# Performance work log

Hardware: AMD Instinct MI355X
Metric: run time of the kernel (lower is better)

## Reference

```python
import jax, jax.numpy as jnp
import numpy as np

NEG_INF = -1e9
B, Q, M, D, H = 8, 512, 512, 1024, 16
S = D // H  # size per head


def rel_shift(x):
    # x: [B, H, Q, R] -> TransformerXL relative shift
    b, h, q, r = x.shape
    x = jnp.pad(x, ((0, 0), (0, 0), (0, 0), (1, 0)))
    x = x.reshape(b, h, r + 1, q)[:, :, 1:, :]
    return x.reshape(b, h, q, r)


def setup_inputs() -> dict:
    key = jax.random.key(0)
    ks = jax.random.split(key, 10)
    query_seqs = jax.random.normal(ks[0], (B, Q, D), jnp.float32)
    memory_seqs = jax.random.normal(ks[1], (B, M, D), jnp.float32)
    positional_encoding = jax.random.normal(ks[2], (Q + M, D), jnp.float32)
    # causal mask over concatenated [memory | query]: query token i may attend
    # to all memory tokens and query tokens <= i. 1 = masked.
    q_idx = jnp.arange(Q)[:, None]
    r_idx = jnp.arange(Q + M)[None, :]
    token_mask = (r_idx > q_idx + M).astype(jnp.float32)[None, None]  # [1,1,Q,Q+M]
    std = 0.02
    Wq = jax.random.normal(ks[3], (D, H, S), jnp.float32) * std
    Wk = jax.random.normal(ks[4], (D, H, S), jnp.float32) * std
    Wv = jax.random.normal(ks[5], (D, H, S), jnp.float32) * std
    Wr = jax.random.normal(ks[6], (D, H, S), jnp.float32) * std
    Wo = jax.random.normal(ks[7], (H, S, D), jnp.float32) * std
    content_bias = jax.random.normal(ks[8], (H, S), jnp.float32) * std
    position_bias = jax.random.normal(ks[9], (H, S), jnp.float32) * std
    return dict(query_seqs=query_seqs, memory_seqs=memory_seqs,
                positional_encoding=positional_encoding, token_mask=token_mask,
                Wq=Wq, Wk=Wk, Wv=Wv, Wr=Wr, Wo=Wo,
                content_bias=content_bias, position_bias=position_bias)


def reference(query_seqs, memory_seqs, positional_encoding, token_mask,
              Wq, Wk, Wv, Wr, Wo, content_bias, position_bias):
    # reference = [memory | query] along time axis
    reference_seqs = jnp.concatenate([memory_seqs, query_seqs], axis=1)  # [B,R,D]
    q = jnp.einsum('bqd,dhs->bqhs', query_seqs, Wq)       # [B,Q,H,S]
    k = jnp.einsum('brd,dhs->brhs', reference_seqs, Wk)   # [B,R,H,S]
    v = jnp.einsum('brd,dhs->brhs', reference_seqs, Wv)   # [B,R,H,S]
    r = jnp.einsum('rd,dhs->rhs', positional_encoding, Wr)  # [R,H,S]

    content = jnp.einsum('bqhs,brhs->bhqr', q + content_bias, k)
    positions = jnp.einsum('bqhs,rhs->bhqr', q + position_bias, r)
    positions = rel_shift(positions)

    logits = (content + positions) / jnp.sqrt(jnp.float32(S))
    logits = logits + token_mask * NEG_INF
    attn = jax.nn.softmax(logits, axis=3)  # dropout disabled (inference)

    out = jnp.einsum('bhqr,brhs->bqhs', attn, v)
    return jnp.einsum('bqhs,hsd->bqd', out, Wo)
```

## Files before the change

kernel.cpp:

```cpp
#include <hip/hip_runtime.h>

typedef _Float16 f16;
typedef _Float16 f16x8 __attribute__((ext_vector_type(8)));
typedef float f32x4 __attribute__((ext_vector_type(4)));

#define MFMA_F16(a, b, c) __builtin_amdgcn_mfma_f32_16x16x32_f16((a), (b), (c), 0, 0, 0)

#define SCL 0.125f

__device__ __forceinline__ void gl_lds16(const void* g, void* l) {
    __builtin_amdgcn_global_load_lds((const __attribute__((address_space(1))) unsigned int*)g,
                                     (__attribute__((address_space(3))) unsigned int*)l, 16, 0, 0);
}

__global__ void prep(const float* __restrict__ q, const float* __restrict__ mem,
                     const float* __restrict__ Wq, const float* __restrict__ Wk,
                     const float* __restrict__ Wv, const float* __restrict__ Wr,
                     const float* __restrict__ Wo,
                     f16* __restrict__ wt, f16* __restrict__ ref16)
{
    __shared__ float t[32][33];
    const int bid = blockIdx.x, tid = threadIdx.x;
    if (bid < 5120) {
        const int wi = bid >> 10, tt = bid & 1023;
        const float* src;
        switch (wi) { case 0: src = Wq; break; case 1: src = Wk; break;
                      case 2: src = Wv; break; case 3: src = Wr; break; default: src = Wo; }
        f16* dst = wt + ((size_t)wi << 20);
        const int x = (tt & 31) * 32, y = (tt >> 5) * 32;
        const int tx = tid & 31, ty = tid >> 5;
#pragma unroll
        for (int k2 = 0; k2 < 4; ++k2)
            t[ty + k2 * 8][tx] = src[(size_t)(y + ty + k2 * 8) * 1024 + x + tx];
        __syncthreads();
#pragma unroll
        for (int k2 = 0; k2 < 4; ++k2)
            dst[(size_t)(x + ty + k2 * 8) * 1024 + y + tx] = (f16)t[tx][ty + k2 * 8];
    } else {
        const int idx = (bid - 5120) * 256 + tid;
        const int half = idx >> 19;
        const int c = idx & 0x7FFFF;
        const int b = c >> 16, i = (c >> 7) & 511, ch = c & 127;
        const float* src = (half == 0 ? q : mem) + (((size_t)(b * 512 + i)) << 10) + ch * 8;
        const int t2 = (half == 0) ? (512 + i) : i;
        f16* dst = ref16 + ((((size_t)b << 10) + t2) << 10) + ch * 8;
        const float4 f0 = reinterpret_cast<const float4*>(src)[0];
        const float4 f1 = reinterpret_cast<const float4*>(src)[1];
        f16x8 v;
        v[0] = (f16)f0.x; v[1] = (f16)f0.y; v[2] = (f16)f0.z; v[3] = (f16)f0.w;
        v[4] = (f16)f1.x; v[5] = (f16)f1.y; v[6] = (f16)f1.z; v[7] = (f16)f1.w;
        *reinterpret_cast<f16x8*>(dst) = v;
    }
}

__global__ __launch_bounds__(256, 4)
void proj_kernel(const f16* __restrict__ ref16, const float* __restrict__ posenc,
                 const f16* __restrict__ wts,
                 f16* __restrict__ qc16, f16* __restrict__ qp16,
                 f16* __restrict__ k16, f16* __restrict__ vT16, f16* __restrict__ r16,
                 const float* __restrict__ cb, const float* __restrict__ pbias)
{
    __shared__ __align__(16) f16 SH[16384];
    f16* At = SH;
    f16* Bt = SH + 8192;

    const int tid = threadIdx.x, lane = tid & 63, w = tid >> 6;
    const int wr = w >> 1, wc = w & 1;

    const int bid = blockIdx.x;
    int mode, local, perx, shf;
    if (bid < 256)       { mode = 0; local = bid;        perx = 4; shf = 2; }
    else if (bid < 768)  { mode = 1; local = bid - 256;  perx = 8; shf = 3; }
    else if (bid < 1280) { mode = 2; local = bid - 768;  perx = 8; shf = 3; }
    else                 { mode = 3; local = bid - 1280; perx = 1; shf = 0; }
    const int xcd = local & 7, m = local >> 3;
    const int rt = xcd * perx + (m & (perx - 1));
    const int ct = m >> shf;
    const int i0 = rt * 128, n0 = ct * 128;
    const f16* BT = wts + ((size_t)mode << 20);

    f32x4 acc[4][4] = {};

    for (int ks = 0; ks < 16; ++ks) {
        const int k0 = ks * 64;
#pragma unroll
        for (int it = 0; it < 4; ++it) {
            const int c = tid + it * 256;
            const int row = c >> 3, ch = c & 7, chs = ch ^ (row & 7);
            const int grow = i0 + row;
            char* lA = reinterpret_cast<char*>(At) + ((c & ~63) << 4);
            char* lB = reinterpret_cast<char*>(Bt) + ((c & ~63) << 4);
            if (mode == 3) {
                const float* sr = posenc + (size_t)grow * 1024 + k0 + ch * 8;
                const float4 f0 = reinterpret_cast<const float4*>(sr)[0];
                const float4 f1 = reinterpret_cast<const float4*>(sr)[1];
                f16x8 av;
                av[0] = (f16)f0.x; av[1] = (f16)f0.y; av[2] = (f16)f0.z; av[3] = (f16)f0.w;
                av[4] = (f16)f1.x; av[5] = (f16)f1.y; av[6] = (f16)f1.z; av[7] = (f16)f1.w;
                *reinterpret_cast<f16x8*>(reinterpret_cast<char*>(At) + row * 128 + (chs << 4)) = av;
            } else {
                const size_t arow = (mode == 0) ? (size_t)((grow >> 9) * 1024 + 512 + (grow & 511))
                                                : (size_t)grow;
                gl_lds16(ref16 + arow * 1024 + k0 + chs * 8, lA);
            }
            gl_lds16(BT + (size_t)(n0 + row) * 1024 + k0 + chs * 8, lB);
        }
        __syncthreads();
#pragma unroll
        for (int kk = 0; kk < 2; ++kk) {
            f16x8 avf[4], bvf[4];
            const int chh = kk * 4 + (lane >> 4);
#pragma unroll
            for (int mi = 0; mi < 4; ++mi) {
                const int row = wr * 64 + mi * 16 + (lane & 15);
                avf[mi] = *reinterpret_cast<const f16x8*>(reinterpret_cast<char*>(At) + row * 128 + ((chh ^ (row & 7)) << 4));
            }
#pragma unroll
            for (int n = 0; n < 4; ++n) {
                const int row = wc * 64 + n * 16 + (lane & 15);
                bvf[n] = *reinterpret_cast<const f16x8*>(reinterpret_cast<char*>(Bt) + row * 128 + ((chh ^ (row & 7)) << 4));
            }
#pragma unroll
            for (int mi = 0; mi < 4; ++mi)
#pragma unroll
                for (int n = 0; n < 4; ++n)
                    acc[mi][n] = MFMA_F16(avf[mi], bvf[n], acc[mi][n]);
        }
        __syncthreads();
    }

    if (mode == 2) {
#pragma unroll
        for (int mi = 0; mi < 4; ++mi)
#pragma unroll
            for (int n = 0; n < 4; ++n)
#pragma unroll
                for (int rg = 0; rg < 4; ++rg) {
                    const int jl = wr * 64 + mi * 16 + (lane >> 4) * 4 + rg;
                    const int cl = wc * 64 + n * 16 + (lane & 15);
                    SH[cl * 128 + jl] = (f16)acc[mi][n][rg];
                }
        __syncthreads();
        const int b = i0 >> 10;
        const int j0l = i0 & 1023;
#pragma unroll
        for (int it = 0; it < 8; ++it) {
            const int c = tid + it * 256;
            const int cl = c >> 4, ch = c & 15;
            const int col = n0 + cl;
            const int h = col >> 6, s = col & 63;
            f16* dst = vT16 + (((size_t)(b * 16 + h) * 64 + s) * 1024 + j0l + ch * 8);
            *reinterpret_cast<f16x8*>(dst) = *reinterpret_cast<const f16x8*>(SH + cl * 128 + ch * 8);
        }
    } else {
#pragma unroll
        for (int mi = 0; mi < 4; ++mi)
#pragma unroll
            for (int n = 0; n < 4; ++n)
#pragma unroll
                for (int rg = 0; rg < 4; ++rg) {
                    const int row = i0 + wr * 64 + mi * 16 + (lane >> 4) * 4 + rg;
                    const int col = n0 + wc * 64 + n * 16 + (lane & 15);
                    const float v = acc[mi][n][rg];
                    if (mode == 0) {
                        const int b = row >> 9, i = row & 511, h = col >> 6, s = col & 63;
                        const size_t idx = (((size_t)(b * 16 + h) * 512) + i) * 64 + s;
                        qc16[idx] = (f16)((v + cb[col]) * SCL);
                        qp16[idx] = (f16)((v + pbias[col]) * SCL);
                    } else if (mode == 1) {
                        const int b = row >> 10, j = row & 1023, h = col >> 6, s = col & 63;
                        k16[(((size_t)(b * 16 + h) * 1024) + j) * 64 + s] = (f16)v;
                    } else {
                        const int h = col >> 6, s = col & 63;
                        r16[((size_t)h * 1024 + row) * 64 + s] = (f16)v;
                    }
                }
    }
}

__global__ __launch_bounds__(256, 4)
void oproj_kernel(const f16* __restrict__ ao16, const f16* __restrict__ WoT, float* __restrict__ out)
{
    __shared__ __align__(16) f16 SH[16384];
    f16* At = SH;
    f16* Bt = SH + 8192;
    const int tid = threadIdx.x, lane = tid & 63, w = tid >> 6;
    const int wr = w >> 1, wc = w & 1;
    const int xcd = blockIdx.x & 7, m = blockIdx.x >> 3;
    const int rt = xcd * 4 + (m & 3), ct = m >> 2;
    const int i0 = rt * 128, n0 = ct * 128;

    f32x4 acc[4][4] = {};
    for (int ks = 0; ks < 16; ++ks) {
        const int k0 = ks * 64;
#pragma unroll
        for (int it = 0; it < 4; ++it) {
            const int c = tid + it * 256;
            const int row = c >> 3, ch = c & 7, chs = ch ^ (row & 7);
            char* lA = reinterpret_cast<char*>(At) + ((c & ~63) << 4);
            char* lB = reinterpret_cast<char*>(Bt) + ((c & ~63) << 4);
            gl_lds16(ao16 + (size_t)(i0 + row) * 1024 + k0 + chs * 8, lA);
            gl_lds16(WoT + (size_t)(n0 + row) * 1024 + k0 + chs * 8, lB);
        }
        __syncthreads();
#pragma unroll
        for (int kk = 0; kk < 2; ++kk) {
            f16x8 avf[4], bvf[4];
            const int chh = kk * 4 + (lane >> 4);
#pragma unroll
            for (int mi = 0; mi < 4; ++mi) {
                const int row = wr * 64 + mi * 16 + (lane & 15);
                avf[mi] = *reinterpret_cast<const f16x8*>(reinterpret_cast<char*>(At) + row * 128 + ((chh ^ (row & 7)) << 4));
            }
#pragma unroll
            for (int n = 0; n < 4; ++n) {
                const int row = wc * 64 + n * 16 + (lane & 15);
                bvf[n] = *reinterpret_cast<const f16x8*>(reinterpret_cast<char*>(Bt) + row * 128 + ((chh ^ (row & 7)) << 4));
            }
#pragma unroll
            for (int mi = 0; mi < 4; ++mi)
#pragma unroll
                for (int n = 0; n < 4; ++n)
                    acc[mi][n] = MFMA_F16(avf[mi], bvf[n], acc[mi][n]);
        }
        __syncthreads();
    }
#pragma unroll
    for (int mi = 0; mi < 4; ++mi)
#pragma unroll
        for (int n = 0; n < 4; ++n)
#pragma unroll
            for (int rg = 0; rg < 4; ++rg) {
                const int row = i0 + wr * 64 + mi * 16 + (lane >> 4) * 4 + rg;
                const int col = n0 + wc * 64 + n * 16 + (lane & 15);
                out[(size_t)row * 1024 + col] = acc[mi][n][rg];
            }
}

__global__ __launch_bounds__(512, 4)
void attn_kernel(const f16* __restrict__ qc16, const f16* __restrict__ qp16,
                 const f16* __restrict__ k16, const f16* __restrict__ vT16,
                 const f16* __restrict__ r16, f16* __restrict__ attnout)
{
    __shared__ __align__(16) f16 KT[4096], VT[4096], RT[4096];
    __shared__ __align__(16) f16 PR[128 * 68];
    __shared__ __align__(16) f16 PB[8 * 2 * 16 * 68];

    const int tid = threadIdx.x, lane = tid & 63, w = tid >> 6;
    const int n = blockIdx.x;
    const int xcd = n & 7, m = n >> 3;
    const int h = xcd + 8 * (m >> 5);
    const int b = (m >> 2) & 7;
    const int iB = m & 3;
    const int i0 = iB * 128;
    const int bh = b * 16 + h;

    const f16* kbase = k16 + (size_t)bh * 1024 * 64;
    const f16* vbase = vT16 + (size_t)bh * 64 * 1024;
    const f16* rbase = r16 + (size_t)h * 1024 * 64;

    f16x8 qcf[2], qpf[2];
    {
        const size_t qoff = ((size_t)bh * 512 + i0 + w * 16 + (lane & 15)) * 64;
#pragma unroll
        for (int kk = 0; kk < 2; ++kk) {
            const int ch = (kk * 4 + (lane >> 4)) * 8;
            qcf[kk] = *reinterpret_cast<const f16x8*>(qc16 + qoff + ch);
            qpf[kk] = *reinterpret_cast<const f16x8*>(qp16 + qoff + ch);
        }
    }

    auto stage64 = [&](f16* dst, const f16* src, int rowstride) {
        const int row = tid >> 3, ch = tid & 7, chs = ch ^ (row & 7);
        gl_lds16(src + (size_t)row * rowstride + chs * 8,
                 reinterpret_cast<char*>(dst) + ((tid & ~63) << 4));
    };

    auto compute_pblock = [&](int bt) {
        const int slot = bt & 1;
        f32x4 pc[4] = {};
#pragma unroll
        for (int kk = 0; kk < 2; ++kk) {
            const int chh = kk * 4 + (lane >> 4);
#pragma unroll
            for (int tf = 0; tf < 4; ++tf) {
                const int brow = tf * 16 + (lane & 15);
                const f16x8 rv = *reinterpret_cast<const f16x8*>(reinterpret_cast<char*>(RT) + brow * 128 + ((chh ^ (brow & 7)) << 4));
                pc[tf] = MFMA_F16(qpf[kk], rv, pc[tf]);
            }
        }
        f16* pbw = PB + (size_t)((w * 2 + slot) * 16) * 68;
#pragma unroll
        for (int tf = 0; tf < 4; ++tf)
#pragma unroll
            for (int rg = 0; rg < 4; ++rg) {
                const int r = (lane >> 4) * 4 + rg;
                pbw[r * 68 + tf * 16 + (lane & 15)] = (f16)pc[tf][rg];
            }
    };

    {
        const int bt0 = 6 - 2 * iB;
        stage64(RT, rbase + (size_t)(bt0 * 64) * 64, 64);
        __syncthreads();
        compute_pblock(bt0);
        __syncthreads();
        stage64(RT, rbase + (size_t)((bt0 + 1) * 64) * 64, 64);
        __syncthreads();
        compute_pblock(bt0 + 1);
    }

    float mrun[4] = {-1e30f, -1e30f, -1e30f, -1e30f};
    float lrun[4] = {0.f, 0.f, 0.f, 0.f};
    f32x4 o[4] = {};

    const int njt = 2 * iB + 10;
    for (int jt = 0; jt < njt; ++jt) {
        const int j0 = jt * 64;
        const int bt = jt - 2 * iB + 8;
        __syncthreads();
        stage64(KT, kbase + (size_t)j0 * 64, 64);
        stage64(VT, vbase + j0, 1024);
        if (bt <= 15) stage64(RT, rbase + (size_t)(bt * 64) * 64, 64);
        __syncthreads();

        if (w < 4 && bt <= 15) compute_pblock(bt);

        f32x4 cfr[4] = {};
        __builtin_amdgcn_s_setprio(1);
#pragma unroll
        for (int kk = 0; kk < 2; ++kk) {
            const int chh = kk * 4 + (lane >> 4);
#pragma unroll
            for (int jf = 0; jf < 4; ++jf) {
                const int brow = jf * 16 + (lane & 15);
                const f16x8 kv = *reinterpret_cast<const f16x8*>(reinterpret_cast<char*>(KT) + brow * 128 + ((chh ^ (brow & 7)) << 4));
                cfr[jf] = MFMA_F16(qcf[kk], kv, cfr[jf]);
            }
        }
        __builtin_amdgcn_s_setprio(0);

        const int tb = j0 + 511 - i0 - w * 16;
        float lg[4][4];
#pragma unroll
        for (int jf = 0; jf < 4; ++jf)
#pragma unroll
            for (int rg = 0; rg < 4; ++rg) {
                const int il = (lane >> 4) * 4 + rg;
                const int t = tb + jf * 16 + (lane & 15) - il;
                const float pv = (float)PB[(size_t)((w * 2 + ((t >> 6) & 1)) * 16 + il) * 68 + (t & 63)];
                lg[jf][rg] = (t <= 1023) ? (cfr[jf][rg] + pv) : -1e30f;
            }

        float mx[4];
#pragma unroll
        for (int rg = 0; rg < 4; ++rg) {
            float v = fmaxf(fmaxf(lg[0][rg], lg[1][rg]), fmaxf(lg[2][rg], lg[3][rg]));
#pragma unroll
            for (int d = 1; d < 16; d <<= 1) v = fmaxf(v, __shfl_xor(v, d));
            mx[rg] = v;
        }
        const float need = fmaxf(fmaxf(mx[0] - mrun[0], mx[1] - mrun[1]),
                                 fmaxf(mx[2] - mrun[2], mx[3] - mrun[3]));
        if (__all(need <= 8.0f)) {
#pragma unroll
            for (int rg = 0; rg < 4; ++rg) {
                float rs = 0.f;
                const int il = w * 16 + (lane >> 4) * 4 + rg;
#pragma unroll
                for (int jf = 0; jf < 4; ++jf) {
                    const float p = __expf(lg[jf][rg] - mrun[rg]);
                    rs += p;
                    PR[il * 68 + jf * 16 + (lane & 15)] = (f16)p;
                }
#pragma unroll
                for (int d = 1; d < 16; d <<= 1) rs += __shfl_xor(rs, d);
                lrun[rg] += rs;
            }
        } else {
#pragma unroll
            for (int rg = 0; rg < 4; ++rg) {
                const float mnew = fmaxf(mrun[rg], mx[rg]);
                const float al = __expf(mrun[rg] - mnew);
                mrun[rg] = mnew;
                float rs = 0.f;
                const int il = w * 16 + (lane >> 4) * 4 + rg;
#pragma unroll
                for (int jf = 0; jf < 4; ++jf) {
                    const float p = __expf(lg[jf][rg] - mnew);
                    rs += p;
                    PR[il * 68 + jf * 16 + (lane & 15)] = (f16)p;
                }
#pragma unroll
                for (int d = 1; d < 16; d <<= 1) rs += __shfl_xor(rs, d);
                lrun[rg] = lrun[rg] * al + rs;
#pragma unroll
                for (int sf = 0; sf < 4; ++sf) o[sf][rg] *= al;
            }
        }

        __builtin_amdgcn_s_setprio(1);
#pragma unroll
        for (int kk = 0; kk < 2; ++kk) {
            const int chh = kk * 4 + (lane >> 4);
            const int arow = w * 16 + (lane & 15);
            const f16x8 ap = *reinterpret_cast<const f16x8*>(reinterpret_cast<char*>(PR) + arow * 136 + chh * 16);
#pragma unroll
            for (int sf = 0; sf < 4; ++sf) {
                const int brow = sf * 16 + (lane & 15);
                const f16x8 vv = *reinterpret_cast<const f16x8*>(reinterpret_cast<char*>(VT) + brow * 128 + ((chh ^ (brow & 7)) << 4));
                o[sf] = MFMA_F16(ap, vv, o[sf]);
            }
        }
        __builtin_amdgcn_s_setprio(0);

        if (w >= 4 && bt <= 15) compute_pblock(bt);
    }

#pragma unroll
    for (int sf = 0; sf < 4; ++sf)
#pragma unroll
        for (int rg = 0; rg < 4; ++rg) {
            const int il = w * 16 + (lane >> 4) * 4 + rg;
            const int row = b * 512 + i0 + il;
            const int col = h * 64 + sf * 16 + (lane & 15);
            attnout[(size_t)row * 1024 + col] = (f16)(o[sf][rg] / lrun[rg]);
        }
}

extern "C" void kernel_launch(void* const* d_in, const int* in_sizes, int n_in,
                              void* d_out, int out_size, void* d_ws, size_t ws_size,
                              hipStream_t stream)
{
    const float* query = (const float*)d_in[0];
    const float* memory = (const float*)d_in[1];
    const float* posenc = (const float*)d_in[2];
    const float* Wq = (const float*)d_in[4];
    const float* Wk = (const float*)d_in[5];
    const float* Wv = (const float*)d_in[6];
    const float* Wr = (const float*)d_in[7];
    const float* Wo = (const float*)d_in[8];
    const float* cb = (const float*)d_in[9];
    const float* pb = (const float*)d_in[10];
    float* out = (float*)d_out;

    if (ws_size < (size_t)38 * (1u << 20) * sizeof(f16)) return;
    f16* ws = (f16*)d_ws;
    f16* WoT = ws + (4u << 20);
    f16* ref16 = ws + (5u << 20);
    f16* ao16 = ref16;
    f16* qc16 = ref16 + (8u << 20);
    f16* qp16 = qc16 + (4u << 20);
    f16* k16 = qp16 + (4u << 20);
    f16* vT16 = k16 + (8u << 20);
    f16* r16 = vT16 + (8u << 20);

    prep<<<9216, 256, 0, stream>>>(query, memory, Wq, Wk, Wv, Wr, Wo, ws, ref16);
    proj_kernel<<<1344, 256, 0, stream>>>(ref16, posenc, ws, qc16, qp16, k16, vT16, r16, cb, pb);
    attn_kernel<<<512, 512, 0, stream>>>(qc16, qp16, k16, vT16, r16, ao16);
    oproj_kernel<<<256, 256, 0, stream>>>(ao16, WoT, out);
}
```

Before: 192.2 us.

## Replace projection GEMMs with 8-wave triple-buffered pipelined 256x128 GEMM kernel

Replaces the 128x128-tile, 4-wave projection and output-projection GEMMs with one 512-thread kernel. It uses 256x128 tiles and a 3-stage LDS ring of async global-to-LDS loads, waited on with explicit vmcnt. Loads for stage t+2 are interleaved with the MFMA work, using barriers and setprio to overlap memory with compute. It also reorders the modes (K, V, Q, R) and reuses the kernel for the output projection. The costs are larger LDS use, lower occupancy, and fewer blocks (128 for the output projection), which may underfill the GPU.

```diff
diff --git a/kernel.cpp b/kernel.cpp
--- a/kernel.cpp
+++ b/kernel.cpp
@@ -7,6 +7,9 @@
 #define MFMA_F16(a, b, c) __builtin_amdgcn_mfma_f32_16x16x32_f16((a), (b), (c), 0, 0, 0)
 
 #define SCL 0.125f
+
+#define VM_WAIT6 asm volatile("s_waitcnt vmcnt(6)" ::: "memory")
+#define VM_WAIT0 asm volatile("s_waitcnt vmcnt(0)" ::: "memory")
 
 __device__ __forceinline__ void gl_lds16(const void* g, void* l) {
     __builtin_amdgcn_global_load_lds((const __attribute__((address_space(1))) unsigned int*)g,
@@ -53,188 +56,210 @@
     }
 }
 
-__global__ __launch_bounds__(256, 4)
-void proj_kernel(const f16* __restrict__ ref16, const float* __restrict__ posenc,
-                 const f16* __restrict__ wts,
-                 f16* __restrict__ qc16, f16* __restrict__ qp16,
-                 f16* __restrict__ k16, f16* __restrict__ vT16, f16* __restrict__ r16,
-                 const float* __restrict__ cb, const float* __restrict__ pbias)
+__global__ __launch_bounds__(512, 2)
+void gemm8p_kernel(const f16* __restrict__ ref16, const float* __restrict__ posenc,
+                   const f16* __restrict__ ao16, const f16* __restrict__ wts,
+                   f16* __restrict__ qc16, f16* __restrict__ qp16,
+                   f16* __restrict__ k16, f16* __restrict__ vT16, f16* __restrict__ r16,
+                   float* __restrict__ out,
+                   const float* __restrict__ cb, const float* __restrict__ pbias,
+                   int is_oproj)
 {
-    __shared__ __align__(16) f16 SH[16384];
-    f16* At = SH;
-    f16* Bt = SH + 8192;
+    __shared__ __align__(16) f16 SH[3 * 24576];
 
     const int tid = threadIdx.x, lane = tid & 63, w = tid >> 6;
-    const int wr = w >> 1, wc = w & 1;
+    const int wm = w >> 2, wn = w & 3;
 
     const int bid = blockIdx.x;
-    int mode, local, perx, shf;
-    if (bid < 256)       { mode = 0; local = bid;        perx = 4; shf = 2; }
-    else if (bid < 768)  { mode = 1; local = bid - 256;  perx = 8; shf = 3; }
-    else if (bid < 1280) { mode = 2; local = bid - 768;  perx = 8; shf = 3; }
-    else                 { mode = 3; local = bid - 1280; perx = 1; shf = 0; }
-    const int xcd = local & 7, m = local >> 3;
-    const int rt = xcd * perx + (m & (perx - 1));
-    const int ct = m >> shf;
-    const int i0 = rt * 128, n0 = ct * 128;
-    const f16* BT = wts + ((size_t)mode << 20);
-
-    f32x4 acc[4][4] = {};
-
-    for (int ks = 0; ks < 16; ++ks) {
-        const int k0 = ks * 64;
-#pragma unroll
-        for (int it = 0; it < 4; ++it) {
-            const int c = tid + it * 256;
+    int mode, local;
+    if (is_oproj)        { mode = 4; local = bid; }
+    else if (bid < 256)  { mode = 0; local = bid; }
+    else if (bid < 512)  { mode = 1; local = bid - 256; }
+    else if (bid < 640)  { mode = 2; local = bid - 512; }
+    else                 { mode = 3; local = bid - 640; }
+    int rt, ct;
+    if (mode == 0 || mode == 1)      { rt = (local & 7) * 4 + ((local >> 3) & 3); ct = local >> 5; }
+    else if (mode == 2 || mode == 4) { rt = (local & 7) * 2 + ((local >> 3) & 1); ct = local >> 4; }
+    else                             { rt = local & 3; ct = local >> 2; }
+    const int i0 = rt * 256, n0 = ct * 128;
+
+    const f16* BT = wts + ((size_t)(mode == 0 ? 1 : mode == 1 ? 2 : mode == 2 ? 0 : mode == 3 ? 3 : 4) << 20);
+    const f16* Ag = (mode == 4) ? ao16 : ref16;
+
+    f32x4 acc[8][2] = {};
+
+    auto stage_q = [&](int t, int q) {
+        if (t > 15) return;
+        f16* Ad = SH + (t % 3) * 24576;
+        f16* Bd = Ad + 16384;
+        const int k0 = t * 64;
+        {
+            const int c = tid + q * 512;
             const int row = c >> 3, ch = c & 7, chs = ch ^ (row & 7);
             const int grow = i0 + row;
-            char* lA = reinterpret_cast<char*>(At) + ((c & ~63) << 4);
-            char* lB = reinterpret_cast<char*>(Bt) + ((c & ~63) << 4);
-            if (mode == 3) {
-                const float* sr = posenc + (size_t)grow * 1024 + k0 + ch * 8;
+            const size_t arow = (mode == 2) ? (size_t)((grow >> 9) * 1024 + 512 + (grow & 511))
+                                            : (size_t)grow;
+            gl_lds16(Ag + arow * 1024 + k0 + chs * 8,
+                     reinterpret_cast<char*>(Ad) + ((c & ~63) << 4));
+        }
+        if (q < 2) {
+            const int c = tid + q * 512;
+            const int row = c >> 3, ch = c & 7, chs = ch ^ (row & 7);
+            gl_lds16(BT + (size_t)(n0 + row) * 1024 + k0 + chs * 8,
+                     reinterpret_cast<char*>(Bd) + ((c & ~63) << 4));
+        }
+    };
+
+    if (mode != 3) {
+#pragma unroll
+        for (int q = 0; q < 4; ++q) stage_q(0, q);
+#pragma unroll
+        for (int q = 0; q < 4; ++q) stage_q(1, q);
+
+        for (int t = 0; t < 16; ++t) {
+            f16* As = SH + (t % 3) * 24576;
+            f16* Bs = As + 16384;
+            if (t < 15) { VM_WAIT6; } else { VM_WAIT0; }
+            __builtin_amdgcn_sched_barrier(0);
+            __builtin_amdgcn_s_barrier();
+            f16x8 bvf[2][2];
+#pragma unroll
+            for (int q = 0; q < 4; ++q) {
+                f16x8 avf[2][2];
+#pragma unroll
+                for (int kk = 0; kk < 2; ++kk) {
+                    const int chh = kk * 4 + (lane >> 4);
+#pragma unroll
+                    for (int d = 0; d < 2; ++d) {
+                        const int row = wm * 128 + (q * 2 + d) * 16 + (lane & 15);
+                        avf[d][kk] = *reinterpret_cast<const f16x8*>(
+                            reinterpret_cast<char*>(As) + row * 128 + ((chh ^ (row & 7)) << 4));
+                    }
+                    if (q == 0) {
+#pragma unroll
+                        for (int n = 0; n < 2; ++n) {
+                            const int row = wn * 32 + n * 16 + (lane & 15);
+                            bvf[n][kk] = *reinterpret_cast<const f16x8*>(
+                                reinterpret_cast<char*>(Bs) + row * 128 + ((chh ^ (row & 7)) << 4));
+                        }
+                    }
+                }
+                stage_q(t + 2, q);
+                __builtin_amdgcn_sched_barrier(0);
+                __builtin_amdgcn_s_barrier();
+                __builtin_amdgcn_s_setprio(1);
+#pragma unroll
+                for (int kk = 0; kk < 2; ++kk)
+#pragma unroll
+                    for (int d = 0; d < 2; ++d)
+#pragma unroll
+                        for (int n = 0; n < 2; ++n)
+                            acc[q * 2 + d][n] = MFMA_F16(avf[d][kk], bvf[n][kk], acc[q * 2 + d][n]);
+                __builtin_amdgcn_s_setprio(0);
+                __builtin_amdgcn_sched_barrier(0);
+                __builtin_amdgcn_s_barrier();
+            }
+        }
+    } else {
+        f16* As = SH;
+        f16* Bs = SH + 16384;
+        for (int t = 0; t < 16; ++t) {
+            const int k0 = t * 64;
+#pragma unroll
+            for (int it = 0; it < 4; ++it) {
+                const int c = tid + it * 512;
+                const int row = c >> 3, ch = c & 7, chs = ch ^ (row & 7);
+                const float* sr = posenc + (size_t)(i0 + row) * 1024 + k0 + ch * 8;
                 const float4 f0 = reinterpret_cast<const float4*>(sr)[0];
                 const float4 f1 = reinterpret_cast<const float4*>(sr)[1];
                 f16x8 av;
                 av[0] = (f16)f0.x; av[1] = (f16)f0.y; av[2] = (f16)f0.z; av[3] = (f16)f0.w;
                 av[4] = (f16)f1.x; av[5] = (f16)f1.y; av[6] = (f16)f1.z; av[7] = (f16)f1.w;
-                *reinterpret_cast<f16x8*>(reinterpret_cast<char*>(At) + row * 128 + (chs << 4)) = av;
-            } else {
-                const size_t arow = (mode == 0) ? (size_t)((grow >> 9) * 1024 + 512 + (grow & 511))
-                                                : (size_t)grow;
-                gl_lds16(ref16 + arow * 1024 + k0 + chs * 8, lA);
-            }
-            gl_lds16(BT + (size_t)(n0 + row) * 1024 + k0 + chs * 8, lB);
-        }
-        __syncthreads();
-#pragma unroll
-        for (int kk = 0; kk < 2; ++kk) {
-            f16x8 avf[4], bvf[4];
-            const int chh = kk * 4 + (lane >> 4);
-#pragma unroll
-            for (int mi = 0; mi < 4; ++mi) {
-                const int row = wr * 64 + mi * 16 + (lane & 15);
-                avf[mi] = *reinterpret_cast<const f16x8*>(reinterpret_cast<char*>(At) + row * 128 + ((chh ^ (row & 7)) << 4));
-            }
-#pragma unroll
-            for (int n = 0; n < 4; ++n) {
-                const int row = wc * 64 + n * 16 + (lane & 15);
-                bvf[n] = *reinterpret_cast<const f16x8*>(reinterpret_cast<char*>(Bt) + row * 128 + ((chh ^ (row & 7)) << 4));
-            }
-#pragma unroll
-            for (int mi = 0; mi < 4; ++mi)
-#pragma unroll
-                for (int n = 0; n < 4; ++n)
-                    acc[mi][n] = MFMA_F16(avf[mi], bvf[n], acc[mi][n]);
-        }
-        __syncthreads();
-    }
-
-    if (mode == 2) {
-#pragma unroll
-        for (int mi = 0; mi < 4; ++mi)
-#pragma unroll
-            for (int n = 0; n < 4; ++n)
+                *reinterpret_cast<f16x8*>(reinterpret_cast<char*>(As) + row * 128 + (chs << 4)) = av;
+            }
+#pragma unroll
+            for (int it = 0; it < 2; ++it) {
+                const int c = tid + it * 512;
+                const int row = c >> 3, ch = c & 7, chs = ch ^ (row & 7);
+                gl_lds16(BT + (size_t)(n0 + row) * 1024 + k0 + chs * 8,
+                         reinterpret_cast<char*>(Bs) + ((c & ~63) << 4));
+            }
+            __syncthreads();
+#pragma unroll
+            for (int kk = 0; kk < 2; ++kk) {
+                const int chh = kk * 4 + (lane >> 4);
+                f16x8 bvf[2];
+#pragma unroll
+                for (int n = 0; n < 2; ++n) {
+                    const int row = wn * 32 + n * 16 + (lane & 15);
+                    bvf[n] = *reinterpret_cast<const f16x8*>(
+                        reinterpret_cast<char*>(Bs) + row * 128 + ((chh ^ (row & 7)) << 4));
+                }
+#pragma unroll
+                for (int mi = 0; mi < 8; ++mi) {
+                    const int row = wm * 128 + mi * 16 + (lane & 15);
+                    const f16x8 av = *reinterpret_cast<const f16x8*>(
+                        reinterpret_cast<char*>(As) + row * 128 + ((chh ^ (row & 7)) << 4));
+#pragma unroll
+                    for (int n = 0; n < 2; ++n)
+                        acc[mi][n] = MFMA_F16(av, bvf[n], acc[mi][n]);
+                }
+            }
+            __syncthreads();
+        }
+    }
+
+    if (mode == 1) {
+        f16* SH2 = SH;
+        __syncthreads();
+#pragma unroll
+        for (int mi = 0; mi < 8; ++mi)
+#pragma unroll
+            for (int n = 0; n < 2; ++n)
 #pragma unroll
                 for (int rg = 0; rg < 4; ++rg) {
-                    const int jl = wr * 64 + mi * 16 + (lane >> 4) * 4 + rg;
-                    const int cl = wc * 64 + n * 16 + (lane & 15);
-                    SH[cl * 128 + jl] = (f16)acc[mi][n][rg];
+                    const int rl = wm * 128 + mi * 16 + (lane >> 4) * 4 + rg;
+                    const int cl = wn * 32 + n * 16 + (lane & 15);
+                    SH2[cl * 264 + rl] = (f16)acc[mi][n][rg];
                 }
         __syncthreads();
         const int b = i0 >> 10;
         const int j0l = i0 & 1023;
 #pragma unroll
         for (int it = 0; it < 8; ++it) {
-            const int c = tid + it * 256;
-            const int cl = c >> 4, ch = c & 15;
+            const int c = tid + it * 512;
+            const int cl = c >> 5, ch = c & 31;
             const int col = n0 + cl;
             const int h = col >> 6, s = col & 63;
             f16* dst = vT16 + (((size_t)(b * 16 + h) * 64 + s) * 1024 + j0l + ch * 8);
-            *reinterpret_cast<f16x8*>(dst) = *reinterpret_cast<const f16x8*>(SH + cl * 128 + ch * 8);
+            *reinterpret_cast<f16x8*>(dst) = *reinterpret_cast<const f16x8*>(SH2 + cl * 264 + ch * 8);
         }
     } else {
 #pragma unroll
-        for (int mi = 0; mi < 4; ++mi)
-#pragma unroll
-            for (int n = 0; n < 4; ++n)
+        for (int mi = 0; mi < 8; ++mi)
+#pragma unroll
+            for (int n = 0; n < 2; ++n)
 #pragma unroll
                 for (int rg = 0; rg < 4; ++rg) {
-                    const int row = i0 + wr * 64 + mi * 16 + (lane >> 4) * 4 + rg;
-                    const int col = n0 + wc * 64 + n * 16 + (lane & 15);
+                    const int row = i0 + wm * 128 + mi * 16 + (lane >> 4) * 4 + rg;
+                    const int col = n0 + wn * 32 + n * 16 + (lane & 15);
                     const float v = acc[mi][n][rg];
                     if (mode == 0) {
+                        const int b = row >> 10, j = row & 1023, h = col >> 6, s = col & 63;
+                        k16[(((size_t)(b * 16 + h) * 1024) + j) * 64 + s] = (f16)v;
+                    } else if (mode == 2) {
                         const int b = row >> 9, i = row & 511, h = col >> 6, s = col & 63;
                         const size_t idx = (((size_t)(b * 16 + h) * 512) + i) * 64 + s;
                         qc16[idx] = (f16)((v + cb[col]) * SCL);
                         qp16[idx] = (f16)((v + pbias[col]) * SCL);
-                    } else if (mode == 1) {
-                        const int b = row >> 10, j = row & 1023, h = col >> 6, s = col & 63;
-                        k16[(((size_t)(b * 16 + h) * 1024) + j) * 64 + s] = (f16)v;
-                    } else {
+                    } else if (mode == 3) {
                         const int h = col >> 6, s = col & 63;
                         r16[((size_t)h * 1024 + row) * 64 + s] = (f16)v;
+                    } else {
+                        out[(size_t)row * 1024 + col] = v;
                     }
                 }
     }
-}
-
-__global__ __launch_bounds__(256, 4)
-void oproj_kernel(const f16* __restrict__ ao16, const f16* __restrict__ WoT, float* __restrict__ out)
-{
-    __shared__ __align__(16) f16 SH[16384];
-    f16* At = SH;
-    f16* Bt = SH + 8192;
-    const int tid = threadIdx.x, lane = tid & 63, w = tid >> 6;
-    const int wr = w >> 1, wc = w & 1;
-    const int xcd = blockIdx.x & 7, m = blockIdx.x >> 3;
-    const int rt = xcd * 4 + (m & 3), ct = m >> 2;
-    const int i0 = rt * 128, n0 = ct * 128;
-
-    f32x4 acc[4][4] = {};
-    for (int ks = 0; ks < 16; ++ks) {
-        const int k0 = ks * 64;
-#pragma unroll
-        for (int it = 0; it < 4; ++it) {
-            const int c = tid + it * 256;
-            const int row = c >> 3, ch = c & 7, chs = ch ^ (row & 7);
-            char* lA = reinterpret_cast<char*>(At) + ((c & ~63) << 4);
-            char* lB = reinterpret_cast<char*>(Bt) + ((c & ~63) << 4);
-            gl_lds16(ao16 + (size_t)(i0 + row) * 1024 + k0 + chs * 8, lA);
-            gl_lds16(WoT + (size_t)(n0 + row) * 1024 + k0 + chs * 8, lB);
-        }
-        __syncthreads();
-#pragma unroll
-        for (int kk = 0; kk < 2; ++kk) {
-            f16x8 avf[4], bvf[4];
-            const int chh = kk * 4 + (lane >> 4);
-#pragma unroll
-            for (int mi = 0; mi < 4; ++mi) {
-                const int row = wr * 64 + mi * 16 + (lane & 15);
-                avf[mi] = *reinterpret_cast<const f16x8*>(reinterpret_cast<char*>(At) + row * 128 + ((chh ^ (row & 7)) << 4));
-            }
-#pragma unroll
-            for (int n = 0; n < 4; ++n) {
-                const int row = wc * 64 + n * 16 + (lane & 15);
-                bvf[n] = *reinterpret_cast<const f16x8*>(reinterpret_cast<char*>(Bt) + row * 128 + ((chh ^ (row & 7)) << 4));
-            }
-#pragma unroll
-            for (int mi = 0; mi < 4; ++mi)
-#pragma unroll
-                for (int n = 0; n < 4; ++n)
-                    acc[mi][n] = MFMA_F16(avf[mi], bvf[n], acc[mi][n]);
-        }
-        __syncthreads();
-    }
-#pragma unroll
-    for (int mi = 0; mi < 4; ++mi)
-#pragma unroll
-        for (int n = 0; n < 4; ++n)
-#pragma unroll
-            for (int rg = 0; rg < 4; ++rg) {
-                const int row = i0 + wr * 64 + mi * 16 + (lane >> 4) * 4 + rg;
-                const int col = n0 + wc * 64 + n * 16 + (lane & 15);
-                out[(size_t)row * 1024 + col] = acc[mi][n][rg];
-            }
 }
 
 __global__ __launch_bounds__(512, 4)
@@ -446,7 +471,6 @@
 
     if (ws_size < (size_t)38 * (1u << 20) * sizeof(f16)) return;
     f16* ws = (f16*)d_ws;
-    f16* WoT = ws + (4u << 20);
     f16* ref16 = ws + (5u << 20);
     f16* ao16 = ref16;
     f16* qc16 = ref16 + (8u << 20);
@@ -456,7 +480,9 @@
     f16* r16 = vT16 + (8u << 20);
 
     prep<<<9216, 256, 0, stream>>>(query, memory, Wq, Wk, Wv, Wr, Wo, ws, ref16);
-    proj_kernel<<<1344, 256, 0, stream>>>(ref16, posenc, ws, qc16, qp16, k16, vT16, r16, cb, pb);
+    gemm8p_kernel<<<672, 512, 0, stream>>>(ref16, posenc, nullptr, ws, qc16, qp16, k16, vT16, r16,
+                                           nullptr, cb, pb, 0);
     attn_kernel<<<512, 512, 0, stream>>>(qc16, qp16, k16, vT16, r16, ao16);
-    oproj_kernel<<<256, 256, 0, stream>>>(ao16, WoT, out);
+    gemm8p_kernel<<<128, 512, 0, stream>>>(ref16, posenc, ao16, ws, qc16, qp16, k16, vT16, r16,
+                                           out, cb, pb, 1);
 }
```

After: 197.9 us. 2.9% more time.
